# Kernel tuning notes

Hardware: AMD Instinct MI355X
Metric: run time of the kernel (lower is better)

The kernel has to match this reference:

```python
import jax, jax.numpy as jnp
import numpy as np

EMBED_DIM = 768
NUM_HEADS = 12
HEAD_DIM = EMBED_DIM // NUM_HEADS


def setup_inputs() -> dict:
    key = jax.random.key(0)
    ks = jax.random.split(key, 5)
    B, N, D = 8, 1024, EMBED_DIM
    s = 1.0 / np.sqrt(D)
    return {
        "x": jax.random.normal(ks[0], (B, N, D), dtype=jnp.float32),
        "qkv_w": jax.random.uniform(ks[1], (D, 3 * D), jnp.float32, -s, s),  # [in, out]
        "qkv_b": jax.random.uniform(ks[2], (3 * D,), jnp.float32, -s, s),
        "proj_w": jax.random.uniform(ks[3], (D, D), jnp.float32, -s, s),
        "proj_b": jax.random.uniform(ks[4], (D,), jnp.float32, -s, s),
    }


def reference(x, qkv_w, qkv_b, proj_w, proj_b):
    B, N, D = x.shape
    H, Hd = NUM_HEADS, HEAD_DIM
    qkv = x @ qkv_w + qkv_b                          # [B, N, 3D]
    qkv = qkv.reshape(B, N, 3, H, Hd)
    q, k, v = (jnp.moveaxis(qkv, 2, 0)[i].transpose(0, 2, 1, 3) for i in range(3))  # each [B, H, N, Hd]
    scores = jnp.einsum("bhnd,bhmd->bhnm", q, k) / np.sqrt(Hd).astype(x.dtype)
    attn = jax.nn.softmax(scores, axis=-1)           # dropout rate 0.0 -> identity
    out = jnp.einsum("bhnm,bhmd->bhnd", attn, v)     # [B, H, N, Hd]
    out = out.transpose(0, 2, 1, 3).reshape(B, N, D)
    return out @ proj_w + proj_b
```

## Files before the change

kernel.cpp:

```cpp
#include <hip/hip_runtime.h>
#include <hip/hip_bf16.h>

typedef __attribute__((ext_vector_type(8))) short short8;
typedef __attribute__((ext_vector_type(4))) float f32x4;
typedef __attribute__((ext_vector_type(2))) unsigned int uint2v;
typedef unsigned int u32;

#define QSCALE 0.1803368801111204f

__device__ inline ushort f2bf(float f) {
    unsigned int i = __builtin_bit_cast(unsigned int, f);
    unsigned int r = (i + 0x7FFFu + ((i >> 16) & 1u)) >> 16;
    return (ushort)r;
}
__device__ inline u32 pack_bf16(float a, float b) {
    float2 f2; f2.x = a; f2.y = b;
    __hip_bfloat162 h = __float22bfloat162_rn(f2);
    u32 r; __builtin_memcpy(&r, &h, 4);
    return r;
}

__device__ __forceinline__ void gload_lds16(const ushort* g, ushort* l) {
    __builtin_amdgcn_global_load_lds(
        (const __attribute__((address_space(1))) u32*)g,
        (__attribute__((address_space(3))) u32*)l, 16, 0, 0);
}

__global__ __launch_bounds__(256) void convert_f32_bf16(
    const float* __restrict__ in, ushort* __restrict__ outp, int n8)
{
    int idx = blockIdx.x * 256 + threadIdx.x;
    if (idx >= n8) return;
    const float4 u0 = *(const float4*)&in[(size_t)idx * 8];
    const float4 u1 = *(const float4*)&in[(size_t)idx * 8 + 4];
    uint2v a, b;
    a.x = pack_bf16(u0.x, u0.y); a.y = pack_bf16(u0.z, u0.w);
    b.x = pack_bf16(u1.x, u1.y); b.y = pack_bf16(u1.z, u1.w);
    *(uint2v*)&outp[(size_t)idx * 8] = a;
    *(uint2v*)&outp[(size_t)idx * 8 + 4] = b;
}

__global__ __launch_bounds__(256) void transpose_f32_bf16(
    const float* __restrict__ W, ushort* __restrict__ Wt, int K, int N)
{
    __shared__ float tile[32][33];
    const int n0 = blockIdx.x * 32;
    const int k0 = blockIdx.y * 32;
    const int tx = threadIdx.x & 31;
    const int ty = threadIdx.x >> 5;
    for (int i = ty; i < 32; i += 8)
        tile[i][tx] = W[(size_t)(k0 + i) * N + n0 + tx];
    __syncthreads();
    for (int i = ty; i < 32; i += 8)
        Wt[(size_t)(n0 + i) * K + k0 + tx] = f2bf(tile[tx][i]);
}

template <bool OUT_FP32, bool QKV_MODE>
__global__ __launch_bounds__(256) void gemm_bt(
    const ushort* __restrict__ A, const ushort* __restrict__ Bt,
    const float* __restrict__ bias, void* __restrict__ C,
    ushort* __restrict__ Vt, int M, int N, int K, int ldc)
{
    __shared__ __attribute__((aligned(16))) ushort As[128][64];
    __shared__ __attribute__((aligned(16))) ushort Bs[128][64];
    const int tid  = threadIdx.x;
    const int lane = tid & 63;
    const int w    = tid >> 6;
    const int wm   = (w >> 1) * 64;
    const int wn   = (w & 1) * 64;
    const int g    = lane >> 4;
    const int t    = lane & 15;
    const int m0   = blockIdx.x * 128;
    const int n0   = blockIdx.y * 128;

    const int lr = lane >> 3;
    const int pc = lane & 7;

    f32x4 acc[4][4];
#pragma unroll
    for (int i = 0; i < 4; i++)
#pragma unroll
        for (int j = 0; j < 4; j++) acc[i][j] = {0.f, 0.f, 0.f, 0.f};

    const int xorc = t & 7;

    for (int k0 = 0; k0 < K; k0 += 64) {
#pragma unroll
        for (int p = 0; p < 4; p++) {
            const int row = w * 32 + p * 8 + lr;
            const int gc  = pc ^ (row & 7);
            gload_lds16(&A[(size_t)(m0 + row) * K + k0 + gc * 8], &As[w * 32 + p * 8][0]);
            gload_lds16(&Bt[(size_t)(n0 + row) * K + k0 + gc * 8], &Bs[w * 32 + p * 8][0]);
        }
        __syncthreads();
#pragma unroll
        for (int s = 0; s < 2; s++) {
            short8 a[4], b[4];
            const int ca = ((s * 4 + g) ^ xorc) * 8;
#pragma unroll
            for (int i = 0; i < 4; i++)
                a[i] = *(const short8*)&As[wm + i * 16 + t][ca];
#pragma unroll
            for (int j = 0; j < 4; j++)
                b[j] = *(const short8*)&Bs[wn + j * 16 + t][ca];
#pragma unroll
            for (int i = 0; i < 4; i++)
#pragma unroll
                for (int j = 0; j < 4; j++)
                    acc[i][j] = __builtin_amdgcn_mfma_f32_16x16x32_bf16(
                        a[i], b[j], acc[i][j], 0, 0, 0);
        }
        __syncthreads();
    }

#pragma unroll
    for (int j = 0; j < 4; j++) {
        int col = n0 + wn + j * 16 + t;
        float bv = bias[col];
        if (QKV_MODE && col >= 1536) {
            int h = (col - 1536) >> 6, d = col & 63;
#pragma unroll
            for (int i = 0; i < 4; i++) {
                int n = m0 + wm + i * 16 + g * 4;
                int bb = n >> 10, nn = n & 1023;
                uint2v u;
                u.x = pack_bf16(acc[i][j][0] + bv, acc[i][j][1] + bv);
                u.y = pack_bf16(acc[i][j][2] + bv, acc[i][j][3] + bv);
                *(uint2v*)&Vt[(((size_t)bb * 12 + h) * 64 + d) * 1024 + nn] = u;
            }
        } else {
#pragma unroll
            for (int i = 0; i < 4; i++)
#pragma unroll
                for (int r = 0; r < 4; r++) {
                    int row = m0 + wm + i * 16 + g * 4 + r;
                    float val = acc[i][j][r] + bv;
                    if (QKV_MODE && col < 768) val *= QSCALE;
                    if (OUT_FP32) ((float*)C)[(size_t)row * ldc + col] = val;
                    else          ((ushort*)C)[(size_t)row * ldc + col] = f2bf(val);
                }
        }
    }
}

__global__ __launch_bounds__(256) void gemm_bt2(
    const ushort* __restrict__ A, const ushort* __restrict__ Bt,
    const float* __restrict__ bias, float* __restrict__ C,
    int M, int N, int K, int ldc)
{
    __shared__ __attribute__((aligned(16))) ushort As[64][64];
    __shared__ __attribute__((aligned(16))) ushort Bs[128][64];
    const int tid  = threadIdx.x;
    const int lane = tid & 63;
    const int w    = tid >> 6;
    const int g    = lane >> 4;
    const int t    = lane & 15;
    const int m0   = blockIdx.x * 64;
    const int n0   = blockIdx.y * 128;
    const int wn   = w * 32;

    const int lr = lane >> 3;
    const int pc = lane & 7;

    f32x4 acc[4][2];
#pragma unroll
    for (int i = 0; i < 4; i++)
#pragma unroll
        for (int j = 0; j < 2; j++) acc[i][j] = {0.f, 0.f, 0.f, 0.f};

    const int xorc = t & 7;

    for (int k0 = 0; k0 < K; k0 += 64) {
#pragma unroll
        for (int p = 0; p < 2; p++) {
            const int row = w * 16 + p * 8 + lr;
            const int gc  = pc ^ (row & 7);
            gload_lds16(&A[(size_t)(m0 + row) * K + k0 + gc * 8], &As[w * 16 + p * 8][0]);
        }
#pragma unroll
        for (int p = 0; p < 4; p++) {
            const int row = w * 32 + p * 8 + lr;
            const int gc  = pc ^ (row & 7);
            gload_lds16(&Bt[(size_t)(n0 + row) * K + k0 + gc * 8], &Bs[w * 32 + p * 8][0]);
        }
        __syncthreads();
#pragma unroll
        for (int s = 0; s < 2; s++) {
            short8 a[4], b[2];
            const int ca = ((s * 4 + g) ^ xorc) * 8;
#pragma unroll
            for (int i = 0; i < 4; i++)
                a[i] = *(const short8*)&As[i * 16 + t][ca];
#pragma unroll
            for (int j = 0; j < 2; j++)
                b[j] = *(const short8*)&Bs[wn + j * 16 + t][ca];
#pragma unroll
            for (int i = 0; i < 4; i++)
#pragma unroll
                for (int j = 0; j < 2; j++)
                    acc[i][j] = __builtin_amdgcn_mfma_f32_16x16x32_bf16(
                        a[i], b[j], acc[i][j], 0, 0, 0);
        }
        __syncthreads();
    }

#pragma unroll
    for (int j = 0; j < 2; j++) {
        int col = n0 + wn + j * 16 + t;
        float bv = bias[col];
#pragma unroll
        for (int i = 0; i < 4; i++)
#pragma unroll
            for (int r = 0; r < 4; r++) {
                int row = m0 + i * 16 + g * 4 + r;
                C[(size_t)row * ldc + col] = acc[i][j][r] + bv;
            }
    }
}

#define PD 72
__global__ __launch_bounds__(256) void attn_kernel(
    const ushort* __restrict__ qk, const ushort* __restrict__ Vt,
    ushort* __restrict__ out)
{
    __shared__ __attribute__((aligned(16))) ushort Ks[2][64][64];
    __shared__ __attribute__((aligned(16))) ushort Vs[2][64][64];
    __shared__ __attribute__((aligned(16))) ushort Ps[4][16][PD];

    const int tid  = threadIdx.x;
    const int lane = tid & 63;
    const int w    = tid >> 6;
    const int g    = lane >> 4;
    const int t    = lane & 15;
    const int bh   = blockIdx.x;
    const int b    = bh / 12;
    const int h    = bh - b * 12;
    const int q0   = blockIdx.y * 128;

    const int srow = tid >> 3;
    const int pc   = tid & 7;
    const size_t base  = (size_t)b * 1024 * 1536;
    const size_t vbase = ((size_t)b * 12 + h) * 64 * 1024;

    short8 qfrag[2][2];
#pragma unroll
    for (int qf = 0; qf < 2; qf++)
#pragma unroll
        for (int s = 0; s < 2; s++)
            qfrag[qf][s] = *(const short8*)&qk[base +
                (size_t)(q0 + qf * 64 + w * 16 + t) * 1536 + h * 64 + s * 32 + g * 8];

#pragma unroll
    for (int p = 0; p < 2; p++) {
        int r = srow + 32 * p;
        int c = (pc ^ (r & 7)) * 8;
        *(short8*)&Ks[0][r][c] =
            *(const short8*)&qk[base + (size_t)r * 1536 + 768 + h * 64 + pc * 8];
        *(short8*)&Vs[0][r][c] =
            *(const short8*)&Vt[vbase + (size_t)r * 1024 + pc * 8];
    }
    __syncthreads();

    f32x4 o_acc[2][4];
#pragma unroll
    for (int qf = 0; qf < 2; qf++)
#pragma unroll
        for (int j = 0; j < 4; j++) o_acc[qf][j] = {0.f, 0.f, 0.f, 0.f};
    float l_part[2] = {0.f, 0.f};

    for (int kt = 0; kt < 16; kt++) {
        const int cur = kt & 1;

        short8 kpre[2], vpre[2];
        if (kt < 15) {
            const int kb = (kt + 1) * 64;
#pragma unroll
            for (int p = 0; p < 2; p++) {
                int r = srow + 32 * p;
                kpre[p] = *(const short8*)&qk[base + (size_t)(kb + r) * 1536 + 768 + h * 64 + pc * 8];
                vpre[p] = *(const short8*)&Vt[vbase + (size_t)r * 1024 + kb + pc * 8];
            }
        }

        short8 kf[2][4], bv[2][4];
#pragma unroll
        for (int s = 0; s < 2; s++)
#pragma unroll
            for (int j = 0; j < 4; j++) {
                const int row = j * 16 + t;
                const int c = ((s * 4 + g) ^ (t & 7)) * 8;
                kf[s][j] = *(const short8*)&Ks[cur][row][c];
                bv[s][j] = *(const short8*)&Vs[cur][row][c];
            }

#pragma unroll
        for (int qf = 0; qf < 2; qf++) {
            f32x4 s_acc[4];
#pragma unroll
            for (int j = 0; j < 4; j++) s_acc[j] = {0.f, 0.f, 0.f, 0.f};
#pragma unroll
            for (int s = 0; s < 2; s++)
#pragma unroll
                for (int j = 0; j < 4; j++)
                    s_acc[j] = __builtin_amdgcn_mfma_f32_16x16x32_bf16(
                        kf[s][j], qfrag[qf][s], s_acc[j], 0, 0, 0);

#pragma unroll
            for (int j = 0; j < 4; j++) {
                float p0 = exp2f(s_acc[j][0]);
                float p1 = exp2f(s_acc[j][1]);
                float p2 = exp2f(s_acc[j][2]);
                float p3 = exp2f(s_acc[j][3]);
                l_part[qf] += (p0 + p1) + (p2 + p3);
                uint2v u;
                u.x = pack_bf16(p0, p1);
                u.y = pack_bf16(p2, p3);
                *(uint2v*)&Ps[w][t][j * 16 + g * 4] = u;
            }

#pragma unroll
            for (int s = 0; s < 2; s++) {
                short8 a = *(const short8*)&Ps[w][t][s * 32 + g * 8];
#pragma unroll
                for (int j = 0; j < 4; j++)
                    o_acc[qf][j] = __builtin_amdgcn_mfma_f32_16x16x32_bf16(
                        a, bv[s][j], o_acc[qf][j], 0, 0, 0);
            }
        }

        if (kt < 15) {
#pragma unroll
            for (int p = 0; p < 2; p++) {
                int r = srow + 32 * p;
                int c = (pc ^ (r & 7)) * 8;
                *(short8*)&Ks[cur ^ 1][r][c] = kpre[p];
                *(short8*)&Vs[cur ^ 1][r][c] = vpre[p];
            }
        }
        __syncthreads();
    }

#pragma unroll
    for (int qf = 0; qf < 2; qf++) {
        float l_tot = l_part[qf];
        l_tot += __shfl_xor(l_tot, 16);
        l_tot += __shfl_xor(l_tot, 32);
        float il[4];
#pragma unroll
        for (int r = 0; r < 4; r++) il[r] = 1.0f / __shfl(l_tot, g * 4 + r);
#pragma unroll
        for (int r = 0; r < 4; r++) {
            int row = q0 + qf * 64 + w * 16 + g * 4 + r;
#pragma unroll
            for (int j = 0; j < 4; j++)
                out[((size_t)(b * 1024 + row)) * 768 + h * 64 + j * 16 + t] =
                    f2bf(o_acc[qf][j][r] * il[r]);
        }
    }
}

extern "C" void kernel_launch(void* const* d_in, const int* in_sizes, int n_in,
                              void* d_out, int out_size, void* d_ws, size_t ws_size,
                              hipStream_t stream)
{
    const float* x      = (const float*)d_in[0];
    const float* qkv_w  = (const float*)d_in[1];
    const float* qkv_b  = (const float*)d_in[2];
    const float* proj_w = (const float*)d_in[3];
    const float* proj_b = (const float*)d_in[4];
    float* out = (float*)d_out;

    char* ws = (char*)d_ws;
    ushort* Wt1 = (ushort*)ws;
    ushort* Wt2 = Wt1 + (size_t)2304 * 768;
    char*   buf = (char*)(Wt2 + (size_t)768 * 768);

    transpose_f32_bf16<<<dim3(72, 24), 256, 0, stream>>>(qkv_w, Wt1, 768, 2304);
    transpose_f32_bf16<<<dim3(24, 24), 256, 0, stream>>>(proj_w, Wt2, 768, 768);

    const size_t wt_bytes   = ((size_t)2304 * 768 + (size_t)768 * 768) * 2;
    const size_t full_bytes = wt_bytes + (size_t)8192 * 768 * 2
                                       + (size_t)8192 * 1536 * 2
                                       + (size_t)8192 * 768 * 2
                                       + (size_t)8192 * 768 * 2;

    if (ws_size >= full_bytes) {
        ushort* xb    = (ushort*)buf;
        ushort* qkO   = xb + (size_t)8192 * 768;
        ushort* VtO   = qkO + (size_t)8192 * 1536;
        ushort* attnO = VtO + (size_t)8192 * 768;
        convert_f32_bf16<<<dim3(3072), 256, 0, stream>>>(x, xb, 786432);
        gemm_bt<false, true><<<dim3(64, 18), 256, 0, stream>>>(
            xb, Wt1, qkv_b, qkO, VtO, 8192, 2304, 768, 1536);
        attn_kernel<<<dim3(96, 8), 256, 0, stream>>>(qkO, VtO, attnO);
        gemm_bt2<<<dim3(128, 6), 256, 0, stream>>>(
            attnO, Wt2, proj_b, out, 8192, 768, 768, 768);
    } else {
        ushort* xbB   = (ushort*)buf;
        ushort* qkB   = xbB + (size_t)1024 * 768;
        ushort* VtB   = qkB + (size_t)1024 * 1536;
        ushort* attnB = VtB + (size_t)1024 * 768;
        for (int b = 0; b < 8; b++) {
            const float* xp = x + (size_t)b * 1024 * 768;
            float* outb = out + (size_t)b * 1024 * 768;
            convert_f32_bf16<<<dim3(384), 256, 0, stream>>>(xp, xbB, 98304);
            gemm_bt<false, true><<<dim3(8, 18), 256, 0, stream>>>(
                xbB, Wt1, qkv_b, qkB, VtB, 1024, 2304, 768, 1536);
            attn_kernel<<<dim3(12, 8), 256, 0, stream>>>(qkB, VtB, attnB);
            gemm_bt2<<<dim3(16, 6), 256, 0, stream>>>(
                attnB, Wt2, proj_b, outb, 1024, 768, 768, 768);
        }
    }
}
```

Before: 196.9 us.

## Shrink attention tiles and use direct global-to-LDS async loads

The attention kernel now handles 64 query rows per block instead of 128 and 32 keys per iteration instead of 64, which doubles the grid and adds a launch bound of 6 blocks per CU to raise occupancy. K and V tiles are fetched with global_load_lds straight into swizzled shared memory, replacing the register-staged prefetch. Smaller tiles cut registers and LDS per block, but each block now pays twice as many barriers and loop iterations, and K/V traffic grows because each block reloads them for fewer queries.

Result: no change. 199.3 us (+1.2%).

```diff
diff --git a/kernel.cpp b/kernel.cpp
--- a/kernel.cpp
+++ b/kernel.cpp
@@ -218,14 +218,13 @@
     }
 }
 
-#define PD 72
-__global__ __launch_bounds__(256) void attn_kernel(
+__global__ __launch_bounds__(256, 6) void attn_kernel(
     const ushort* __restrict__ qk, const ushort* __restrict__ Vt,
     ushort* __restrict__ out)
 {
-    __shared__ __attribute__((aligned(16))) ushort Ks[2][64][64];
-    __shared__ __attribute__((aligned(16))) ushort Vs[2][64][64];
-    __shared__ __attribute__((aligned(16))) ushort Ps[4][16][PD];
+    __shared__ __attribute__((aligned(16))) ushort Ks[2][32][64];
+    __shared__ __attribute__((aligned(16))) ushort Vs[2][64][32];
+    __shared__ __attribute__((aligned(16))) ushort Ps[4][16][40];
 
     const int tid  = threadIdx.x;
     const int lane = tid & 63;
@@ -235,127 +234,90 @@
     const int bh   = blockIdx.x;
     const int b    = bh / 12;
     const int h    = bh - b * 12;
-    const int q0   = blockIdx.y * 128;
-
-    const int srow = tid >> 3;
-    const int pc   = tid & 7;
+    const int q0   = blockIdx.y * 64;
+
     const size_t base  = (size_t)b * 1024 * 1536;
     const size_t vbase = ((size_t)b * 12 + h) * 64 * 1024;
 
-    short8 qfrag[2][2];
-#pragma unroll
-    for (int qf = 0; qf < 2; qf++)
+    const int kr  = lane >> 3;
+    const int kc  = lane & 7;
+    const int kgc = kc ^ kr;
+    const int vr  = lane >> 2;
+    const int vc  = lane & 3;
+    const int vgc = vc ^ (vr & 3);
+
+    const ushort* kg = &qk[base + 768 + (size_t)h * 64 + (size_t)(w * 8 + kr) * 1536 + kgc * 8];
+    const ushort* vg = &Vt[vbase + (size_t)(w * 16 + vr) * 1024 + vgc * 8];
+
+    short8 qfrag[2];
+#pragma unroll
+    for (int s = 0; s < 2; s++)
+        qfrag[s] = *(const short8*)&qk[base + (size_t)(q0 + w * 16 + t) * 1536 +
+                                       h * 64 + s * 32 + g * 8];
+
+    gload_lds16(kg, &Ks[0][w * 8][0]);
+    gload_lds16(vg, &Vs[0][w * 16][0]);
+
+    f32x4 o_acc[4];
+#pragma unroll
+    for (int j = 0; j < 4; j++) o_acc[j] = {0.f, 0.f, 0.f, 0.f};
+    float l_part = 0.f;
+
+    for (int kt = 0; kt < 32; kt++) {
+        const int cur = kt & 1;
+        __syncthreads();
+
+        if (kt < 31) {
+            const int kb = (kt + 1) * 32;
+            gload_lds16(kg + (size_t)kb * 1536, &Ks[cur ^ 1][w * 8][0]);
+            gload_lds16(vg + kb, &Vs[cur ^ 1][w * 16][0]);
+        }
+
+        f32x4 s_acc[2];
+#pragma unroll
+        for (int j = 0; j < 2; j++) s_acc[j] = {0.f, 0.f, 0.f, 0.f};
 #pragma unroll
         for (int s = 0; s < 2; s++)
-            qfrag[qf][s] = *(const short8*)&qk[base +
-                (size_t)(q0 + qf * 64 + w * 16 + t) * 1536 + h * 64 + s * 32 + g * 8];
-
-#pragma unroll
-    for (int p = 0; p < 2; p++) {
-        int r = srow + 32 * p;
-        int c = (pc ^ (r & 7)) * 8;
-        *(short8*)&Ks[0][r][c] =
-            *(const short8*)&qk[base + (size_t)r * 1536 + 768 + h * 64 + pc * 8];
-        *(short8*)&Vs[0][r][c] =
-            *(const short8*)&Vt[vbase + (size_t)r * 1024 + pc * 8];
-    }
-    __syncthreads();
-
-    f32x4 o_acc[2][4];
-#pragma unroll
-    for (int qf = 0; qf < 2; qf++)
-#pragma unroll
-        for (int j = 0; j < 4; j++) o_acc[qf][j] = {0.f, 0.f, 0.f, 0.f};
-    float l_part[2] = {0.f, 0.f};
-
-    for (int kt = 0; kt < 16; kt++) {
-        const int cur = kt & 1;
-
-        short8 kpre[2], vpre[2];
-        if (kt < 15) {
-            const int kb = (kt + 1) * 64;
-#pragma unroll
-            for (int p = 0; p < 2; p++) {
-                int r = srow + 32 * p;
-                kpre[p] = *(const short8*)&qk[base + (size_t)(kb + r) * 1536 + 768 + h * 64 + pc * 8];
-                vpre[p] = *(const short8*)&Vt[vbase + (size_t)r * 1024 + kb + pc * 8];
+#pragma unroll
+            for (int j = 0; j < 2; j++) {
+                short8 kf = *(const short8*)&Ks[cur][j * 16 + t][(((s * 4 + g) ^ (t & 7))) * 8];
+                s_acc[j] = __builtin_amdgcn_mfma_f32_16x16x32_bf16(kf, qfrag[s], s_acc[j], 0, 0, 0);
             }
-        }
-
-        short8 kf[2][4], bv[2][4];
-#pragma unroll
-        for (int s = 0; s < 2; s++)
-#pragma unroll
-            for (int j = 0; j < 4; j++) {
-                const int row = j * 16 + t;
-                const int c = ((s * 4 + g) ^ (t & 7)) * 8;
-                kf[s][j] = *(const short8*)&Ks[cur][row][c];
-                bv[s][j] = *(const short8*)&Vs[cur][row][c];
-            }
-
-#pragma unroll
-        for (int qf = 0; qf < 2; qf++) {
-            f32x4 s_acc[4];
-#pragma unroll
-            for (int j = 0; j < 4; j++) s_acc[j] = {0.f, 0.f, 0.f, 0.f};
-#pragma unroll
-            for (int s = 0; s < 2; s++)
-#pragma unroll
-                for (int j = 0; j < 4; j++)
-                    s_acc[j] = __builtin_amdgcn_mfma_f32_16x16x32_bf16(
-                        kf[s][j], qfrag[qf][s], s_acc[j], 0, 0, 0);
-
-#pragma unroll
-            for (int j = 0; j < 4; j++) {
-                float p0 = exp2f(s_acc[j][0]);
-                float p1 = exp2f(s_acc[j][1]);
-                float p2 = exp2f(s_acc[j][2]);
-                float p3 = exp2f(s_acc[j][3]);
-                l_part[qf] += (p0 + p1) + (p2 + p3);
-                uint2v u;
-                u.x = pack_bf16(p0, p1);
-                u.y = pack_bf16(p2, p3);
-                *(uint2v*)&Ps[w][t][j * 16 + g * 4] = u;
-            }
-
-#pragma unroll
-            for (int s = 0; s < 2; s++) {
-                short8 a = *(const short8*)&Ps[w][t][s * 32 + g * 8];
-#pragma unroll
-                for (int j = 0; j < 4; j++)
-                    o_acc[qf][j] = __builtin_amdgcn_mfma_f32_16x16x32_bf16(
-                        a, bv[s][j], o_acc[qf][j], 0, 0, 0);
-            }
-        }
-
-        if (kt < 15) {
-#pragma unroll
-            for (int p = 0; p < 2; p++) {
-                int r = srow + 32 * p;
-                int c = (pc ^ (r & 7)) * 8;
-                *(short8*)&Ks[cur ^ 1][r][c] = kpre[p];
-                *(short8*)&Vs[cur ^ 1][r][c] = vpre[p];
-            }
-        }
-        __syncthreads();
-    }
-
-#pragma unroll
-    for (int qf = 0; qf < 2; qf++) {
-        float l_tot = l_part[qf];
-        l_tot += __shfl_xor(l_tot, 16);
-        l_tot += __shfl_xor(l_tot, 32);
-        float il[4];
-#pragma unroll
-        for (int r = 0; r < 4; r++) il[r] = 1.0f / __shfl(l_tot, g * 4 + r);
-#pragma unroll
-        for (int r = 0; r < 4; r++) {
-            int row = q0 + qf * 64 + w * 16 + g * 4 + r;
-#pragma unroll
-            for (int j = 0; j < 4; j++)
-                out[((size_t)(b * 1024 + row)) * 768 + h * 64 + j * 16 + t] =
-                    f2bf(o_acc[qf][j][r] * il[r]);
-        }
+
+#pragma unroll
+        for (int j = 0; j < 2; j++) {
+            float p0 = exp2f(s_acc[j][0]);
+            float p1 = exp2f(s_acc[j][1]);
+            float p2 = exp2f(s_acc[j][2]);
+            float p3 = exp2f(s_acc[j][3]);
+            l_part += (p0 + p1) + (p2 + p3);
+            uint2v u;
+            u.x = pack_bf16(p0, p1);
+            u.y = pack_bf16(p2, p3);
+            *(uint2v*)&Ps[w][t][j * 16 + g * 4] = u;
+        }
+
+        short8 a = *(const short8*)&Ps[w][t][g * 8];
+#pragma unroll
+        for (int j = 0; j < 4; j++) {
+            short8 bv = *(const short8*)&Vs[cur][j * 16 + t][(g ^ (t & 3)) * 8];
+            o_acc[j] = __builtin_amdgcn_mfma_f32_16x16x32_bf16(a, bv, o_acc[j], 0, 0, 0);
+        }
+    }
+
+    float l_tot = l_part;
+    l_tot += __shfl_xor(l_tot, 16);
+    l_tot += __shfl_xor(l_tot, 32);
+    float il[4];
+#pragma unroll
+    for (int r = 0; r < 4; r++) il[r] = 1.0f / __shfl(l_tot, g * 4 + r);
+#pragma unroll
+    for (int r = 0; r < 4; r++) {
+        int row = q0 + w * 16 + g * 4 + r;
+#pragma unroll
+        for (int j = 0; j < 4; j++)
+            out[((size_t)(b * 1024 + row)) * 768 + h * 64 + j * 16 + t] =
+                f2bf(o_acc[j][r] * il[r]);
     }
 }
 
@@ -392,7 +354,7 @@
         convert_f32_bf16<<<dim3(3072), 256, 0, stream>>>(x, xb, 786432);
         gemm_bt<false, true><<<dim3(64, 18), 256, 0, stream>>>(
             xb, Wt1, qkv_b, qkO, VtO, 8192, 2304, 768, 1536);
-        attn_kernel<<<dim3(96, 8), 256, 0, stream>>>(qkO, VtO, attnO);
+        attn_kernel<<<dim3(96, 16), 256, 0, stream>>>(qkO, VtO, attnO);
         gemm_bt2<<<dim3(128, 6), 256, 0, stream>>>(
             attnO, Wt2, proj_b, out, 8192, 768, 768, 768);
     } else {
@@ -406,7 +368,7 @@
             convert_f32_bf16<<<dim3(384), 256, 0, stream>>>(xp, xbB, 98304);
             gemm_bt<false, true><<<dim3(8, 18), 256, 0, stream>>>(
                 xbB, Wt1, qkv_b, qkB, VtB, 1024, 2304, 768, 1536);
-            attn_kernel<<<dim3(12, 8), 256, 0, stream>>>(qkB, VtB, attnB);
+            attn_kernel<<<dim3(12, 16), 256, 0, stream>>>(qkB, VtB, attnB);
             gemm_bt2<<<dim3(16, 6), 256, 0, stream>>>(
                 attnB, Wt2, proj_b, outb, 1024, 768, 768, 768);
         }
```
